# Kernel tuning notes

Measured on AMD Instinct MI355X. Metric: run time of the kernel, lower is better.

Reference implementation:

```python
import jax, jax.numpy as jnp
import numpy as np

N = 100000
IN_C, HID_C, OUT_C = 256, 128, 2
E = 3200000


def setup_inputs() -> dict:
    key = jax.random.key(0)
    ks = jax.random.split(key, 8)
    x = jax.random.normal(ks[0], (N, IN_C), dtype=jnp.float32)
    edge_index = jax.random.randint(ks[1], (2, E), 0, N, dtype=jnp.int64)
    edge_weight = jax.random.uniform(ks[2], (E,), dtype=jnp.float32)
    # GCNConv params (Glorot-ish init)
    W1 = jax.random.normal(ks[3], (IN_C, HID_C), dtype=jnp.float32) / np.sqrt(IN_C)
    b1 = jnp.zeros((HID_C,), dtype=jnp.float32)
    W2 = jax.random.normal(ks[4], (HID_C, OUT_C), dtype=jnp.float32) / np.sqrt(HID_C)
    b2 = jnp.zeros((OUT_C,), dtype=jnp.float32)
    return {"x": x, "edge_index": edge_index, "edge_weight": edge_weight,
            "W1": W1, "b1": b1, "W2": W2, "b2": b2}


def _gcn_norm(edge_index, edge_weight, num_nodes):
    # Add self-loops with weight 1 (PyG GCNConv default), then symmetric norm.
    loop = jnp.arange(num_nodes, dtype=edge_index.dtype)
    src = jnp.concatenate([edge_index[0], loop])
    dst = jnp.concatenate([edge_index[1], loop])
    w = jnp.concatenate([edge_weight, jnp.ones((num_nodes,), edge_weight.dtype)])
    deg = jax.ops.segment_sum(w, dst, num_segments=num_nodes)
    dinv = jnp.where(deg > 0, jax.lax.rsqrt(deg), 0.0)
    norm = dinv[src] * w * dinv[dst]
    return src, dst, norm


def _gcn_conv(x, src, dst, norm, W, b):
    h = x @ W                                   # [N, C_out] dense transform first
    msg = norm[:, None] * h[src]                # [E+N, C_out] gather + scale
    agg = jax.ops.segment_sum(msg, dst, num_segments=x.shape[0])
    return agg + b


def reference(x, edge_index, edge_weight, W1, b1, W2, b2):
    src, dst, norm = _gcn_norm(edge_index, edge_weight, x.shape[0])
    h = jax.nn.relu(_gcn_conv(x, src, dst, norm, W1, b1))
    # dropout p=0.5 is identity in eval mode
    out = _gcn_conv(h, src, dst, norm, W2, b2)
    return out
```

## Files before the change

### kernel.cpp

```cpp
#include <hip/hip_runtime.h>

#define IN_C  256
#define HID_C 128
#define OUT_C 2
#define BSH   5
#define NB    32
#define BCAP  2048

typedef __attribute__((ext_vector_type(8))) short short8;
typedef __attribute__((ext_vector_type(4))) float float4v;

__device__ __forceinline__ unsigned short f2bf(float f) {
    unsigned u = __float_as_uint(f);
    unsigned r = 0x7fffu + ((u >> 16) & 1u);
    return (unsigned short)((u + r) >> 16);
}
__device__ __forceinline__ unsigned pk2(float a, float b) {
    return (unsigned)f2bf(a) | ((unsigned)f2bf(b) << 16);
}

__global__ void k_wT(const float* __restrict__ W1, unsigned short* __restrict__ w1t) {
    int i = blockIdx.x * 256 + threadIdx.x;
    if (i >= HID_C * IN_C) return;
    int c = i >> 8, k = i & 255;
    w1t[i] = f2bf(W1[(size_t)k * HID_C + c]);
}

__global__ __launch_bounds__(256) void k_count(const int* __restrict__ ei,
                                               int* __restrict__ gcnt,
                                               int E, int K, int W, int CHv) {
    extern __shared__ int lh[];
    int w = blockIdx.x, t = threadIdx.x;
    for (int b = t; b < K; b += 256) lh[b] = 0;
    __syncthreads();
    int j0 = w * CHv;
    int j1 = min(j0 + CHv, E);
    for (int j = j0 + t; j < j1; j += 256)
        atomicAdd(&lh[ei[E + j] >> BSH], 1);
    __syncthreads();
    for (int b = t; b < K; b += 256) gcnt[(size_t)b * W + w] = lh[b];
}

__global__ __launch_bounds__(256) void k_scanA4(const int* __restrict__ cnt,
                                                int* __restrict__ excl,
                                                int* __restrict__ bsum, int n) {
    __shared__ int ss[256];
    int t = threadIdx.x;
    int base = blockIdx.x * 4096 + t * 16;
    int v[16]; int s = 0;
#pragma unroll
    for (int q = 0; q < 16; q++) { v[q] = (base + q < n) ? cnt[base + q] : 0; s += v[q]; }
    ss[t] = s;
    __syncthreads();
    for (int d = 1; d < 256; d <<= 1) {
        int x = (t >= d) ? ss[t - d] : 0;
        __syncthreads();
        ss[t] += x;
        __syncthreads();
    }
    int pre = (t == 0) ? 0 : ss[t - 1];
    if (t == 255) bsum[blockIdx.x] = ss[255];
    int run = pre;
#pragma unroll
    for (int q = 0; q < 16; q++) { if (base + q < n) excl[base + q] = run; run += v[q]; }
}

__global__ __launch_bounds__(256) void k_scanB(int* __restrict__ bsum, int nb) {
    __shared__ int ss[256];
    int t = threadIdx.x;
    int v = (t < nb) ? bsum[t] : 0;
    ss[t] = v;
    __syncthreads();
    for (int d = 1; d < 256; d <<= 1) {
        int x = (t >= d) ? ss[t - d] : 0;
        __syncthreads();
        ss[t] += x;
        __syncthreads();
    }
    if (t < nb) bsum[t] = ss[t] - v;
}

__global__ void k_scanC4(int* __restrict__ gpos, const int* __restrict__ bsum, int n) {
    int i = blockIdx.x * 256 + threadIdx.x;
    if (i < n) gpos[i] += bsum[i >> 12];
}

__global__ __launch_bounds__(256) void k_place(const int* __restrict__ ei,
                                               const float* __restrict__ w,
                                               const int* __restrict__ gpos,
                                               int2* __restrict__ ebuf,
                                               int E, int K, int W, int CHv) {
    extern __shared__ int lc[];
    int wg = blockIdx.x, t = threadIdx.x;
    for (int b = t; b < K; b += 256) lc[b] = gpos[(size_t)b * W + wg];
    __syncthreads();
    int j0 = wg * CHv;
    int j1 = min(j0 + CHv, E);
    for (int j = j0 + t; j < j1; j += 256) {
        int s = ei[j], d = ei[E + j];
        float wv = w[j];
        int pos = atomicAdd(&lc[d >> BSH], 1);
        ebuf[pos] = make_int2(s | ((d & (NB - 1)) << 17), __float_as_int(wv));
    }
}

__global__ __launch_bounds__(256) void k_bucket(const int2* __restrict__ ebuf,
                                                const int* __restrict__ gpos,
                                                int2* __restrict__ edata,
                                                int* __restrict__ rowptr,
                                                float* __restrict__ dinv,
                                                int W, int K, int E, int N) {
    __shared__ int2 le[BCAP], ls[BCAP];
    __shared__ int lh[NB], lex[NB], lc[NB];
    int b = blockIdx.x, t = threadIdx.x;
    int base = gpos[(size_t)b * W];
    int next = (b + 1 < K) ? gpos[(size_t)(b + 1) * W] : E;
    int cnt = next - base;
    if (t < NB) lh[t] = 0;
    __syncthreads();
    if (cnt <= BCAP) {
        for (int j = t; j < cnt; j += 256) {
            int2 e = ebuf[base + j];
            le[j] = e;
            atomicAdd(&lh[(e.x >> 17) & (NB - 1)], 1);
        }
        __syncthreads();
        if (t == 0) {
            int run = 0;
            for (int i = 0; i < NB; i++) { lex[i] = run; lc[i] = run; run += lh[i]; }
        }
        __syncthreads();
        for (int j = t; j < cnt; j += 256) {
            int2 e = le[j];
            int pos = atomicAdd(&lc[(e.x >> 17) & (NB - 1)], 1);
            ls[pos] = make_int2(e.x & 0x1FFFF, e.y);
        }
        __syncthreads();
        for (int j = t; j < cnt; j += 256) edata[base + j] = ls[j];
        if (t < NB) {
            int node = b * NB + t;
            if (node < N) {
                rowptr[node] = base + lex[t];
                float s = 1.0f;
                int rb = lex[t], re = rb + lh[t];
                for (int j = rb; j < re; j++) s += __int_as_float(ls[j].y);
                dinv[node] = s > 0.f ? rsqrtf(s) : 0.f;
            }
        }
    } else {
        for (int j = base + t; j < next; j += 256)
            atomicAdd(&lh[(ebuf[j].x >> 17) & (NB - 1)], 1);
        __syncthreads();
        if (t == 0) {
            int run = 0;
            for (int i = 0; i < NB; i++) { lex[i] = run; lc[i] = run; run += lh[i]; }
        }
        __syncthreads();
        for (int j = base + t; j < next; j += 256) {
            int2 e = ebuf[j];
            int pos = base + atomicAdd(&lc[(e.x >> 17) & (NB - 1)], 1);
            edata[pos] = make_int2(e.x & 0x1FFFF, e.y);
        }
        __syncthreads();
        if (t < NB) {
            int node = b * NB + t;
            if (node < N) {
                int rb = base + lex[t], re = rb + lh[t];
                rowptr[node] = rb;
                float s = 1.0f;
                for (int j = rb; j < re; j++) s += __int_as_float(edata[j].y);
                dinv[node] = s > 0.f ? rsqrtf(s) : 0.f;
            }
        }
    }
    if (b == K - 1 && t == 0) rowptr[N] = E;
}

__global__ void k_scale(int2* __restrict__ edata, const float* __restrict__ dinv, int E) {
    int i = blockIdx.x * 256 + threadIdx.x;
    if (i >= E) return;
    int2 e = edata[i];
    e.y = __float_as_int(__int_as_float(e.y) * dinv[e.x]);
    edata[i] = e;
}

#define XS_LD 36
#define WT_LD 260
__global__ __launch_bounds__(256) void k_gemm1(const float* __restrict__ x,
                                               const unsigned short* __restrict__ w1t,
                                               unsigned short* __restrict__ h1b, int n) {
    __shared__ __align__(16) unsigned short wt[HID_C * WT_LD];
    __shared__ __align__(16) unsigned short xs[64 * XS_LD];
    int tid  = threadIdx.x;
    int row0 = blockIdx.x * 64;
    for (int it = 0; it < 16; it++) {
        int idx = it * 256 + tid;
        int c = idx >> 5, kc = idx & 31;
        uint4 v = *(const uint4*)(w1t + (size_t)c * IN_C + kc * 8);
        uint2* dst = (uint2*)(wt + c * WT_LD + kc * 8);
        dst[0] = make_uint2(v.x, v.y);
        dst[1] = make_uint2(v.z, v.w);
    }
    int wv = tid >> 6, ln = tid & 63;
    int m = ln & 15, quad = ln >> 4;
    float4v acc[8];
#pragma unroll
    for (int ct = 0; ct < 8; ct++) acc[ct] = (float4v){0.f, 0.f, 0.f, 0.f};

    for (int k0 = 0; k0 < IN_C; k0 += 32) {
        __syncthreads();
        {
            int r = tid >> 2, s4 = tid & 3;
            int gr = row0 + r; if (gr >= n) gr = n - 1;
            const float4* px = (const float4*)(x + (size_t)gr * IN_C + k0 + s4 * 8);
            float4 a = px[0], bq = px[1];
            uint2* d = (uint2*)(xs + r * XS_LD + s4 * 8);
            d[0] = make_uint2(pk2(a.x, a.y), pk2(a.z, a.w));
            d[1] = make_uint2(pk2(bq.x, bq.y), pk2(bq.z, bq.w));
        }
        __syncthreads();
        union { uint2 u[2]; short8 v; } af;
        const uint2* pa = (const uint2*)(xs + (wv * 16 + m) * XS_LD + quad * 8);
        af.u[0] = pa[0]; af.u[1] = pa[1];
#pragma unroll
        for (int ct = 0; ct < 8; ct++) {
            union { uint2 u[2]; short8 v; } bf;
            const uint2* pb = (const uint2*)(wt + (ct * 16 + m) * WT_LD + k0 + quad * 8);
            bf.u[0] = pb[0]; bf.u[1] = pb[1];
            acc[ct] = __builtin_amdgcn_mfma_f32_16x16x32_bf16(af.v, bf.v, acc[ct], 0, 0, 0);
        }
    }
    __syncthreads();
    unsigned short* ot = wt;
#pragma unroll
    for (int ct = 0; ct < 8; ct++)
#pragma unroll
        for (int r = 0; r < 4; r++)
            ot[(wv * 16 + quad * 4 + r) * 136 + ct * 16 + m] = f2bf(acc[ct][r]);
    __syncthreads();
#pragma unroll
    for (int p = 0; p < 4; p++) {
        int idx = p * 256 + tid;
        int r = idx >> 4, c8 = idx & 15;
        if (row0 + r < n)
            *(uint4*)(h1b + (size_t)(row0 + r) * HID_C + c8 * 8) =
                *(const uint4*)(ot + r * 136 + c8 * 8);
    }
}

__global__ __launch_bounds__(256) void k_agg1(const int* __restrict__ rowptr,
                                              const int2* __restrict__ edata,
                                              const unsigned short* __restrict__ h1b,
                                              const float* __restrict__ dinv,
                                              const float* __restrict__ b1,
                                              const float* __restrict__ W2,
                                              float* __restrict__ h2, int n) {
    int wid  = (blockIdx.x * 256 + threadIdx.x) >> 6;
    int lane = threadIdx.x & 63;
    if (wid >= n) return;
    int beg = rowptr[wid], end = rowptr[wid + 1];
    float ax = 0.f, ay = 0.f;
    int j = beg;
    for (; j + 16 <= end; j += 16) {
        int2 e[16];
        unsigned p[16];
#pragma unroll
        for (int q = 0; q < 16; q++) e[q] = edata[j + q];
#pragma unroll
        for (int q = 0; q < 16; q++)
            p[q] = *((const unsigned*)(h1b + (size_t)e[q].x * HID_C) + lane);
#pragma unroll
        for (int q = 0; q < 16; q++) {
            float nm = __int_as_float(e[q].y);
            ax = fmaf(nm, __uint_as_float(p[q] << 16), ax);
            ay = fmaf(nm, __uint_as_float(p[q] & 0xffff0000u), ay);
        }
    }
    for (; j + 4 <= end; j += 4) {
        int2 e[4];
        unsigned p[4];
#pragma unroll
        for (int q = 0; q < 4; q++) e[q] = edata[j + q];
#pragma unroll
        for (int q = 0; q < 4; q++)
            p[q] = *((const unsigned*)(h1b + (size_t)e[q].x * HID_C) + lane);
#pragma unroll
        for (int q = 0; q < 4; q++) {
            float nm = __int_as_float(e[q].y);
            ax = fmaf(nm, __uint_as_float(p[q] << 16), ax);
            ay = fmaf(nm, __uint_as_float(p[q] & 0xffff0000u), ay);
        }
    }
    for (; j < end; j++) {
        int2 e0 = edata[j];
        unsigned p0 = *((const unsigned*)(h1b + (size_t)e0.x * HID_C) + lane);
        float nm = __int_as_float(e0.y);
        ax = fmaf(nm, __uint_as_float(p0 << 16), ax);
        ay = fmaf(nm, __uint_as_float(p0 & 0xffff0000u), ay);
    }
    float di = dinv[wid]; float sc = di * di;
    unsigned ps = *((const unsigned*)(h1b + (size_t)wid * HID_C) + lane);
    float2 bv = ((const float2*)b1)[lane];
    float ox = bv.x + sc * __uint_as_float(ps << 16)         + di * ax;
    float oy = bv.y + sc * __uint_as_float(ps & 0xffff0000u) + di * ay;
    ox = fmaxf(ox, 0.f);
    oy = fmaxf(oy, 0.f);
    float4 w4 = *((const float4*)(W2 + 4 * lane));
    float s0 = ox * w4.x + oy * w4.z;
    float s1 = ox * w4.y + oy * w4.w;
#pragma unroll
    for (int d = 32; d > 0; d >>= 1) {
        s0 += __shfl_xor(s0, d);
        s1 += __shfl_xor(s1, d);
    }
    if (lane == 0)
        ((float2*)h2)[wid] = make_float2(s0, s1);
}

__global__ __launch_bounds__(256) void k_agg2(const int* __restrict__ rowptr,
                                              const int2* __restrict__ edata,
                                              const float* __restrict__ h2,
                                              const float* __restrict__ dinv,
                                              const float* __restrict__ b2,
                                              float* __restrict__ out, int n) {
    int wid  = (blockIdx.x * 256 + threadIdx.x) >> 6;
    int lane = threadIdx.x & 63;
    if (wid >= n) return;
    int beg = rowptr[wid], end = rowptr[wid + 1];
    float sx = 0.f, sy = 0.f;
    for (int j = beg + lane; j < end; j += 64) {
        int2 ed = edata[j];
        float nm = __int_as_float(ed.y);
        float2 v = ((const float2*)h2)[ed.x];
        sx = fmaf(nm, v.x, sx);
        sy = fmaf(nm, v.y, sy);
    }
#pragma unroll
    for (int d = 32; d > 0; d >>= 1) {
        sx += __shfl_xor(sx, d);
        sy += __shfl_xor(sy, d);
    }
    if (lane == 0) {
        float di = dinv[wid]; float sc = di * di;
        float2 hv = ((const float2*)h2)[wid];
        ((float2*)out)[wid] = make_float2(b2[0] + sc * hv.x + di * sx,
                                          b2[1] + sc * hv.y + di * sy);
    }
}

extern "C" void kernel_launch(void* const* d_in, const int* in_sizes, int n_in,
                              void* d_out, int out_size, void* d_ws, size_t ws_size,
                              hipStream_t stream) {
    const float* x  = (const float*)d_in[0];
    const int*   ei = (const int*)d_in[1];
    const float* ew = (const float*)d_in[2];
    const float* W1 = (const float*)d_in[3];
    const float* b1 = (const float*)d_in[4];
    const float* W2 = (const float*)d_in[5];
    const float* b2 = (const float*)d_in[6];
    float* out = (float*)d_out;

    int N = in_sizes[0] / IN_C;
    int E = in_sizes[2];
    int K = (N + NB - 1) >> BSH;
    int W = 256;
    int CHv = (E + W - 1) / W;
    int KW = K * W;

    char* ws = (char*)d_ws;
    float* dinv   = (float*)ws; ws += (size_t)N * 4;
    int*   rowptr = (int*)ws;   ws += (size_t)(N + 1) * 4 + 4;
    int*   gcnt   = (int*)ws;   ws += (size_t)KW * 4;
    int*   bsum   = (int*)ws;   ws += 1024;
    int2*  ebuf   = (int2*)ws;  ws += (size_t)E * 8;
    int2*  edata  = (int2*)ws;  ws += (size_t)E * 8;
    unsigned short* w1t = (unsigned short*)ws; ws += (size_t)HID_C * IN_C * 2;
    unsigned short* h1b = (unsigned short*)ws; ws += (size_t)N * HID_C * 2;
    float* h2     = (float*)ws; ws += (size_t)N * OUT_C * 4;

    int nb_e  = (E + 255) / 256;
    int nb_s4 = (KW + 4095) / 4096;
    int nb_sc = (KW + 255) / 256;
    int nb_w  = (N * 64 + 255) / 256;
    size_t lds_k = (size_t)K * 4;

    k_wT    <<<(HID_C * IN_C + 255) / 256, 256, 0, stream>>>(W1, w1t);
    k_count <<<W, 256, lds_k, stream>>>(ei, gcnt, E, K, W, CHv);
    k_scanA4<<<nb_s4, 256, 0, stream>>>(gcnt, gcnt, bsum, KW);
    k_scanB <<<1, 256, 0, stream>>>(bsum, nb_s4);
    k_scanC4<<<nb_sc, 256, 0, stream>>>(gcnt, bsum, KW);
    k_place <<<W, 256, lds_k, stream>>>(ei, ew, gcnt, ebuf, E, K, W, CHv);
    k_bucket<<<K, 256, 0, stream>>>(ebuf, gcnt, edata, rowptr, dinv, W, K, E, N);
    k_scale <<<nb_e, 256, 0, stream>>>(edata, dinv, E);
    k_gemm1 <<<(N + 63) / 64, 256, 0, stream>>>(x, w1t, h1b, N);
    k_agg1  <<<nb_w, 256, 0, stream>>>(rowptr, edata, h1b, dinv, b1, W2, h2, N);
    k_agg2  <<<nb_w, 256, 0, stream>>>(rowptr, edata, h2, dinv, b2, out, N);
}
```

Measured before the change: 532.2 us.

## Pack CSR edges into 32-bit records with fp16 weight and widen buckets

Edge records in the CSR change from int2 (src, fp32 weight) to one 32-bit word: a 17-bit source index and a 15-bit fp16 weight with the sign bit dropped. This halves the edge-stream bytes read by both aggregation kernels and the scale kernel. Bucket width also grows from 32 to 128 nodes, so fewer k_bucket blocks run and the k_count/k_place LDS histograms shrink. Weights and norms now carry fp16 precision, which adds rounding error. Bucket sizes near 128*32 edges approach the 6144-edge LDS cap, so more buckets may fall to the slow global path.

```diff
diff --git a/kernel.cpp b/kernel.cpp
--- a/kernel.cpp
+++ b/kernel.cpp
@@ -1,11 +1,12 @@
 #include <hip/hip_runtime.h>
+#include <hip/hip_fp16.h>
 
 #define IN_C  256
 #define HID_C 128
 #define OUT_C 2
-#define BSH   5
-#define NB    32
-#define BCAP  2048
+#define BSH   7
+#define NB    128
+#define BCAP  6144
 
 typedef __attribute__((ext_vector_type(8))) short short8;
 typedef __attribute__((ext_vector_type(4))) float float4v;
@@ -17,6 +18,16 @@
 }
 __device__ __forceinline__ unsigned pk2(float a, float b) {
     return (unsigned)f2bf(a) | ((unsigned)f2bf(b) << 16);
+}
+__device__ __forceinline__ unsigned enc_edge(int src, float w) {
+    unsigned h = (unsigned)(__half_as_ushort(__float2half(w)) & 0x7FFF);
+    return (h << 17) | (unsigned)src;
+}
+__device__ __forceinline__ void dec_edge(unsigned rec, int& s, float& w) {
+    s = (int)(rec & 0x1FFFFu);
+    __half hh;
+    *(unsigned short*)&hh = (unsigned short)(rec >> 17);
+    w = __half2float(hh);
 }
 
 __global__ void k_wT(const float* __restrict__ W1, unsigned short* __restrict__ w1t) {
@@ -106,24 +117,21 @@
 
 __global__ __launch_bounds__(256) void k_bucket(const int2* __restrict__ ebuf,
                                                 const int* __restrict__ gpos,
-                                                int2* __restrict__ edata,
+                                                unsigned* __restrict__ epack,
                                                 int* __restrict__ rowptr,
                                                 float* __restrict__ dinv,
                                                 int W, int K, int E, int N) {
-    __shared__ int2 le[BCAP], ls[BCAP];
+    __shared__ int2 ls[BCAP];
     __shared__ int lh[NB], lex[NB], lc[NB];
     int b = blockIdx.x, t = threadIdx.x;
     int base = gpos[(size_t)b * W];
     int next = (b + 1 < K) ? gpos[(size_t)(b + 1) * W] : E;
     int cnt = next - base;
-    if (t < NB) lh[t] = 0;
+    for (int i = t; i < NB; i += 256) lh[i] = 0;
     __syncthreads();
     if (cnt <= BCAP) {
-        for (int j = t; j < cnt; j += 256) {
-            int2 e = ebuf[base + j];
-            le[j] = e;
-            atomicAdd(&lh[(e.x >> 17) & (NB - 1)], 1);
-        }
+        for (int j = t; j < cnt; j += 256)
+            atomicAdd(&lh[(ebuf[base + j].x >> 17) & (NB - 1)], 1);
         __syncthreads();
         if (t == 0) {
             int run = 0;
@@ -131,18 +139,21 @@
         }
         __syncthreads();
         for (int j = t; j < cnt; j += 256) {
-            int2 e = le[j];
+            int2 e = ebuf[base + j];
             int pos = atomicAdd(&lc[(e.x >> 17) & (NB - 1)], 1);
             ls[pos] = make_int2(e.x & 0x1FFFF, e.y);
         }
         __syncthreads();
-        for (int j = t; j < cnt; j += 256) edata[base + j] = ls[j];
-        if (t < NB) {
-            int node = b * NB + t;
+        for (int j = t; j < cnt; j += 256) {
+            int2 e = ls[j];
+            epack[base + j] = enc_edge(e.x, __int_as_float(e.y));
+        }
+        for (int r = t; r < NB; r += 256) {
+            int node = b * NB + r;
             if (node < N) {
-                rowptr[node] = base + lex[t];
+                rowptr[node] = base + lex[r];
                 float s = 1.0f;
-                int rb = lex[t], re = rb + lh[t];
+                int rb = lex[r], re = rb + lh[r];
                 for (int j = rb; j < re; j++) s += __int_as_float(ls[j].y);
                 dinv[node] = s > 0.f ? rsqrtf(s) : 0.f;
             }
@@ -159,16 +170,20 @@
         for (int j = base + t; j < next; j += 256) {
             int2 e = ebuf[j];
             int pos = base + atomicAdd(&lc[(e.x >> 17) & (NB - 1)], 1);
-            edata[pos] = make_int2(e.x & 0x1FFFF, e.y);
-        }
-        __syncthreads();
-        if (t < NB) {
-            int node = b * NB + t;
+            epack[pos] = enc_edge(e.x & 0x1FFFF, __int_as_float(e.y));
+        }
+        __syncthreads();
+        for (int r = t; r < NB; r += 256) {
+            int node = b * NB + r;
             if (node < N) {
-                int rb = base + lex[t], re = rb + lh[t];
+                int rb = base + lex[r], re = rb + lh[r];
                 rowptr[node] = rb;
                 float s = 1.0f;
-                for (int j = rb; j < re; j++) s += __int_as_float(edata[j].y);
+                for (int j = rb; j < re; j++) {
+                    int ss; float wv;
+                    dec_edge(epack[j], ss, wv);
+                    s += wv;
+                }
                 dinv[node] = s > 0.f ? rsqrtf(s) : 0.f;
             }
         }
@@ -176,12 +191,13 @@
     if (b == K - 1 && t == 0) rowptr[N] = E;
 }
 
-__global__ void k_scale(int2* __restrict__ edata, const float* __restrict__ dinv, int E) {
+__global__ void k_scale(unsigned* __restrict__ epack, const float* __restrict__ dinv, int E) {
     int i = blockIdx.x * 256 + threadIdx.x;
     if (i >= E) return;
-    int2 e = edata[i];
-    e.y = __float_as_int(__int_as_float(e.y) * dinv[e.x]);
-    edata[i] = e;
+    unsigned rec = epack[i];
+    int src; float wv;
+    dec_edge(rec, src, wv);
+    epack[i] = enc_edge(src, wv * dinv[src]);
 }
 
 #define XS_LD 36
@@ -249,7 +265,7 @@
 }
 
 __global__ __launch_bounds__(256) void k_agg1(const int* __restrict__ rowptr,
-                                              const int2* __restrict__ edata,
+                                              const unsigned* __restrict__ epack,
                                               const unsigned short* __restrict__ h1b,
                                               const float* __restrict__ dinv,
                                               const float* __restrict__ b1,
@@ -262,41 +278,39 @@
     float ax = 0.f, ay = 0.f;
     int j = beg;
     for (; j + 16 <= end; j += 16) {
-        int2 e[16];
+        int   es[16]; float ew[16];
         unsigned p[16];
 #pragma unroll
-        for (int q = 0; q < 16; q++) e[q] = edata[j + q];
+        for (int q = 0; q < 16; q++) dec_edge(epack[j + q], es[q], ew[q]);
 #pragma unroll
         for (int q = 0; q < 16; q++)
-            p[q] = *((const unsigned*)(h1b + (size_t)e[q].x * HID_C) + lane);
+            p[q] = *((const unsigned*)(h1b + (size_t)es[q] * HID_C) + lane);
 #pragma unroll
         for (int q = 0; q < 16; q++) {
-            float nm = __int_as_float(e[q].y);
-            ax = fmaf(nm, __uint_as_float(p[q] << 16), ax);
-            ay = fmaf(nm, __uint_as_float(p[q] & 0xffff0000u), ay);
+            ax = fmaf(ew[q], __uint_as_float(p[q] << 16), ax);
+            ay = fmaf(ew[q], __uint_as_float(p[q] & 0xffff0000u), ay);
         }
     }
     for (; j + 4 <= end; j += 4) {
-        int2 e[4];
+        int   es[4]; float ew[4];
         unsigned p[4];
 #pragma unroll
-        for (int q = 0; q < 4; q++) e[q] = edata[j + q];
+        for (int q = 0; q < 4; q++) dec_edge(epack[j + q], es[q], ew[q]);
 #pragma unroll
         for (int q = 0; q < 4; q++)
-            p[q] = *((const unsigned*)(h1b + (size_t)e[q].x * HID_C) + lane);
+            p[q] = *((const unsigned*)(h1b + (size_t)es[q] * HID_C) + lane);
 #pragma unroll
         for (int q = 0; q < 4; q++) {
-            float nm = __int_as_float(e[q].y);
-            ax = fmaf(nm, __uint_as_float(p[q] << 16), ax);
-            ay = fmaf(nm, __uint_as_float(p[q] & 0xffff0000u), ay);
+            ax = fmaf(ew[q], __uint_as_float(p[q] << 16), ax);
+            ay = fmaf(ew[q], __uint_as_float(p[q] & 0xffff0000u), ay);
         }
     }
     for (; j < end; j++) {
-        int2 e0 = edata[j];
-        unsigned p0 = *((const unsigned*)(h1b + (size_t)e0.x * HID_C) + lane);
-        float nm = __int_as_float(e0.y);
-        ax = fmaf(nm, __uint_as_float(p0 << 16), ax);
-        ay = fmaf(nm, __uint_as_float(p0 & 0xffff0000u), ay);
+        int es; float ewv;
+        dec_edge(epack[j], es, ewv);
+        unsigned p0 = *((const unsigned*)(h1b + (size_t)es * HID_C) + lane);
+        ax = fmaf(ewv, __uint_as_float(p0 << 16), ax);
+        ay = fmaf(ewv, __uint_as_float(p0 & 0xffff0000u), ay);
     }
     float di = dinv[wid]; float sc = di * di;
     unsigned ps = *((const unsigned*)(h1b + (size_t)wid * HID_C) + lane);
@@ -318,7 +332,7 @@
 }
 
 __global__ __launch_bounds__(256) void k_agg2(const int* __restrict__ rowptr,
-                                              const int2* __restrict__ edata,
+                                              const unsigned* __restrict__ epack,
                                               const float* __restrict__ h2,
                                               const float* __restrict__ dinv,
                                               const float* __restrict__ b2,
@@ -329,9 +343,9 @@
     int beg = rowptr[wid], end = rowptr[wid + 1];
     float sx = 0.f, sy = 0.f;
     for (int j = beg + lane; j < end; j += 64) {
-        int2 ed = edata[j];
-        float nm = __int_as_float(ed.y);
-        float2 v = ((const float2*)h2)[ed.x];
+        int es; float nm;
+        dec_edge(epack[j], es, nm);
+        float2 v = ((const float2*)h2)[es];
         sx = fmaf(nm, v.x, sx);
         sy = fmaf(nm, v.y, sy);
     }
@@ -373,7 +387,7 @@
     int*   gcnt   = (int*)ws;   ws += (size_t)KW * 4;
     int*   bsum   = (int*)ws;   ws += 1024;
     int2*  ebuf   = (int2*)ws;  ws += (size_t)E * 8;
-    int2*  edata  = (int2*)ws;  ws += (size_t)E * 8;
+    unsigned* epack = (unsigned*)ws; ws += (size_t)E * 4;
     unsigned short* w1t = (unsigned short*)ws; ws += (size_t)HID_C * IN_C * 2;
     unsigned short* h1b = (unsigned short*)ws; ws += (size_t)N * HID_C * 2;
     float* h2     = (float*)ws; ws += (size_t)N * OUT_C * 4;
@@ -390,9 +404,9 @@
     k_scanB <<<1, 256, 0, stream>>>(bsum, nb_s4);
     k_scanC4<<<nb_sc, 256, 0, stream>>>(gcnt, bsum, KW);
     k_place <<<W, 256, lds_k, stream>>>(ei, ew, gcnt, ebuf, E, K, W, CHv);
-    k_bucket<<<K, 256, 0, stream>>>(ebuf, gcnt, edata, rowptr, dinv, W, K, E, N);
-    k_scale <<<nb_e, 256, 0, stream>>>(edata, dinv, E);
+    k_bucket<<<K, 256, 0, stream>>>(ebuf, gcnt, epack, rowptr, dinv, W, K, E, N);
+    k_scale <<<nb_e, 256, 0, stream>>>(epack, dinv, E);
     k_gemm1 <<<(N + 63) / 64, 256, 0, stream>>>(x, w1t, h1b, N);
-    k_agg1  <<<nb_w, 256, 0, stream>>>(rowptr, edata, h1b, dinv, b1, W2, h2, N);
-    k_agg2  <<<nb_w, 256, 0, stream>>>(rowptr, edata, h2, dinv, b2, out, N);
-}
+    k_agg1  <<<nb_w, 256, 0, stream>>>(rowptr, epack, h1b, dinv, b1, W2, h2, N);
+    k_agg2  <<<nb_w, 256, 0, stream>>>(rowptr, epack, h2, dinv, b2, out, N);
+}
```

After: 501.7 us. 1.06x faster.
